# Performance work log

Measured on AMD Instinct MI355X. Metric: run time of the kernel, lower is better.

The kernel has to match this reference:

```python
import jax, jax.numpy as jnp
import numpy as np


def setup_inputs() -> dict:
    key = jax.random.key(0)
    k1, k2 = jax.random.split(key)
    B, Cin, H, W = 32, 32, 128, 128
    Cout, K = 64, 3
    inp = jax.random.normal(k1, (B, Cin, H, W), dtype=jnp.float32)
    # Original stores out_c*in_c*k*k scalar params; equivalent dense weight [Cout, Cin, K, K]
    kernel = jax.random.normal(k2, (Cout, Cin, K, K), dtype=jnp.float32)
    return {"input": inp, "kernel": kernel}


def reference(input, kernel):
    # Stride-1 cross-correlation with 'same' zero padding of (K-1)//2, identical
    # to the nested-loop slice/multiply/sum in the torch module.
    K = kernel.shape[-1]
    pad = (K - 1) // 2
    out = jax.lax.conv_general_dilated(
        input, kernel,
        window_strides=(1, 1),
        padding=[(pad, pad), (pad, pad)],
        dimension_numbers=("NCHW", "OIHW", "NCHW"),
    )
    return out  # [B, Cout, H, W]
```

## Files before the change

### kernel.cpp

```cpp
#include <hip/hip_runtime.h>
#include <hip/hip_bf16.h>
#include <stdint.h>

typedef short bf16x8 __attribute__((ext_vector_type(8)));
typedef float f32x4  __attribute__((ext_vector_type(4)));

#define B_   32
#define CIN  32
#define COUT 64
#define H_   128
#define W_   128
#define HW   (H_ * W_)
#define T_   2
#define RROWS 4
#define PXW  130
#define SCW  68

#define WAIT_LGKM0() __builtin_amdgcn_s_waitcnt(0xC07F)

static __device__ __forceinline__ ushort f2bf(float v) {
    __hip_bfloat16 h = __float2bfloat16(v);
    return __builtin_bit_cast(ushort, h);
}

__global__ void prep_w_kernel(const float* __restrict__ wt, ushort* __restrict__ Wp) {
    int p = blockIdx.x * blockDim.x + threadIdx.x;
    if (p >= COUT * CIN * 9) return;
    int j    = p & 7;
    int lane = (p >> 3) & 63;
    int g    = (p >> 9) & 3;
    int tap  = p >> 11;
    int oc   = g * 16 + (lane & 15);
    int cin  = (lane >> 4) * 8 + j;
    int ky   = tap / 3;
    int kx   = tap % 3;
    Wp[p] = f2bf(wt[(((size_t)oc * CIN + cin) * 3 + ky) * 3 + kx]);
}

__global__ __launch_bounds__(256, 4) void conv_fused_kernel(
    const float* __restrict__ in, const ushort* __restrict__ Wp,
    float* __restrict__ out) {
    __shared__ ushort lds[RROWS * PXW * 32];

    int hw_blk  = blockIdx.x;
    int logical = (hw_blk & 7) * 256 + (hw_blk >> 3);
    int b   = logical >> 6;
    int h0  = (logical & 63) * T_;
    int tid = threadIdx.x;

    for (int i = tid; i < RROWS * PXW; i += 256) {
        int r  = i / PXW;
        int px = i - r * PXW;
        int gy = h0 + r - 1;
        bf16x8 v[4];
        if (gy >= 0 && gy < H_ && px >= 1 && px <= W_) {
            const float* src = in + ((size_t)b * CIN * H_ + gy) * W_ + (px - 1);
#pragma unroll
            for (int q = 0; q < 4; ++q)
#pragma unroll
                for (int j = 0; j < 8; ++j)
                    v[q][j] = (short)f2bf(src[(size_t)(q * 8 + j) * HW]);
        } else {
#pragma unroll
            for (int q = 0; q < 4; ++q)
#pragma unroll
                for (int j = 0; j < 8; ++j)
                    v[q][j] = 0;
        }
        uint32_t base_byte = (uint32_t)i * 64;
        uint32_t sw = ((uint32_t)(px >> 1) & 3u) << 4;
#pragma unroll
        for (int q = 0; q < 4; ++q)
            *(bf16x8*)((char*)lds + base_byte + (((uint32_t)q << 4) ^ sw)) = v[q];
    }
    __syncthreads();

    int wid  = tid >> 6;
    int lane = tid & 63;
    int llo  = lane & 15;
    int lhi  = lane >> 4;
    int row  = wid >> 1;
    int px0  = (wid & 1) * 64;
    int h    = h0 + row;

    f32x4 acc[4][4];
#pragma unroll
    for (int g = 0; g < 4; ++g)
#pragma unroll
        for (int nf = 0; nf < 4; ++nf) {
            acc[g][nf][0] = 0.f; acc[g][nf][1] = 0.f;
            acc[g][nf][2] = 0.f; acc[g][nf][3] = 0.f;
        }

#pragma unroll
    for (int tap = 0; tap < 9; ++tap) {
        int dy = tap / 3;
        int dx = tap % 3;
        int rbase = (row + dy) * PXW;
        bf16x8 Af[4];
#pragma unroll
        for (int g = 0; g < 4; ++g)
            Af[g] = *(const bf16x8*)(Wp + ((size_t)(tap * 4 + g) * 64 + lane) * 8);
#pragma unroll
        for (int nf = 0; nf < 4; ++nf) {
            int px = px0 + nf * 16 + llo + dx;
            uint32_t byte = (uint32_t)(rbase + px) * 64u +
                            (((uint32_t)lhi << 4) ^ ((((uint32_t)px >> 1) & 3u) << 4));
            bf16x8 Bf = *(const bf16x8*)((const char*)lds + byte);
#pragma unroll
            for (int g = 0; g < 4; ++g)
                acc[g][nf] = __builtin_amdgcn_mfma_f32_16x16x32_bf16(Af[g], Bf, acc[g][nf], 0, 0, 0);
        }
    }

    __syncthreads();

    float* myscr = (float*)lds + wid * 16 * SCW;
    float* obase = out + (size_t)b * COUT * HW + (size_t)h * W_ + px0;
#pragma unroll
    for (int g = 0; g < 4; ++g) {
#pragma unroll
        for (int nf = 0; nf < 4; ++nf)
#pragma unroll
            for (int r = 0; r < 4; ++r)
                myscr[(lhi * 4 + r) * SCW + nf * 16 + llo] = acc[g][nf][r];
        WAIT_LGKM0();
#pragma unroll
        for (int j = 0; j < 4; ++j) {
            int ocp = j * 4 + lhi;
            f32x4 vv = *(const f32x4*)(myscr + ocp * SCW + llo * 4);
            int oc = g * 16 + ocp;
            *(f32x4*)(obase + (size_t)oc * HW + llo * 4) = vv;
        }
        WAIT_LGKM0();
    }
}

__global__ void conv_naive_kernel(const float* __restrict__ in,
                                  const float* __restrict__ wt,
                                  float* __restrict__ out) {
    int idx = blockIdx.x * blockDim.x + threadIdx.x;
    if (idx >= B_ * COUT * HW) return;
    int w  = idx & 127;
    int h  = (idx >> 7) & 127;
    int oc = (idx >> 14) & 63;
    int b  = idx >> 20;
    float s = 0.f;
    for (int c = 0; c < CIN; ++c)
        for (int ky = 0; ky < 3; ++ky) {
            int y = h + ky - 1;
            if ((unsigned)y >= (unsigned)H_) continue;
            for (int kx = 0; kx < 3; ++kx) {
                int x = w + kx - 1;
                if ((unsigned)x >= (unsigned)W_) continue;
                s += in[((size_t)(b * CIN + c) * H_ + y) * W_ + x] *
                     wt[(((size_t)oc * CIN + c) * 3 + ky) * 3 + kx];
            }
        }
    out[idx] = s;
}

extern "C" void kernel_launch(void* const* d_in, const int* in_sizes, int n_in,
                              void* d_out, int out_size, void* d_ws, size_t ws_size,
                              hipStream_t stream) {
    const float* in = (const float*)d_in[0];
    const float* wt = (const float*)d_in[1];
    float* out = (float*)d_out;

    size_t Wp_bytes = (size_t)COUT * CIN * 9 * 2;

    if (ws_size >= Wp_bytes) {
        ushort* Wp = (ushort*)d_ws;
        prep_w_kernel<<<(COUT * CIN * 9 + 255) / 256, 256, 0, stream>>>(wt, Wp);
        conv_fused_kernel<<<B_ * (H_ / T_), 256, 0, stream>>>(in, Wp, out);
    } else {
        int total = B_ * COUT * HW;
        conv_naive_kernel<<<(total + 255) / 256, 256, 0, stream>>>(in, wt, out);
    }
}
```

Measured before the change: 50.12 us.

## Give each wave a private LDS halo tile and drop block barriers

After: 51.84 us. +3.4%, slower.

```diff
diff --git a/kernel.cpp b/kernel.cpp
--- a/kernel.cpp
+++ b/kernel.cpp
@@ -11,9 +11,9 @@
 #define H_   128
 #define W_   128
 #define HW   (H_ * W_)
-#define T_   2
-#define RROWS 4
-#define PXW  130
+#define WCOLS 66
+#define WROWS 3
+#define WLDS  (WROWS * WCOLS * 32)
 #define SCW  68
 
 #define WAIT_LGKM0() __builtin_amdgcn_s_waitcnt(0xC07F)
@@ -37,51 +37,80 @@
     Wp[p] = f2bf(wt[(((size_t)oc * CIN + cin) * 3 + ky) * 3 + kx]);
 }
 
-__global__ __launch_bounds__(256, 4) void conv_fused_kernel(
+__global__ __launch_bounds__(256, 4) void conv_wave_kernel(
     const float* __restrict__ in, const ushort* __restrict__ Wp,
     float* __restrict__ out) {
-    __shared__ ushort lds[RROWS * PXW * 32];
+    __shared__ ushort lds[4 * WLDS];
 
     int hw_blk  = blockIdx.x;
     int logical = (hw_blk & 7) * 256 + (hw_blk >> 3);
-    int b   = logical >> 6;
-    int h0  = (logical & 63) * T_;
-    int tid = threadIdx.x;
-
-    for (int i = tid; i < RROWS * PXW; i += 256) {
-        int r  = i / PXW;
-        int px = i - r * PXW;
-        int gy = h0 + r - 1;
-        bf16x8 v[4];
-        if (gy >= 0 && gy < H_ && px >= 1 && px <= W_) {
-            const float* src = in + ((size_t)b * CIN * H_ + gy) * W_ + (px - 1);
-#pragma unroll
-            for (int q = 0; q < 4; ++q)
-#pragma unroll
-                for (int j = 0; j < 8; ++j)
-                    v[q][j] = (short)f2bf(src[(size_t)(q * 8 + j) * HW]);
-        } else {
-#pragma unroll
-            for (int q = 0; q < 4; ++q)
-#pragma unroll
-                for (int j = 0; j < 8; ++j)
-                    v[q][j] = 0;
-        }
-        uint32_t base_byte = (uint32_t)i * 64;
-        uint32_t sw = ((uint32_t)(px >> 1) & 3u) << 4;
-#pragma unroll
-        for (int q = 0; q < 4; ++q)
-            *(bf16x8*)((char*)lds + base_byte + (((uint32_t)q << 4) ^ sw)) = v[q];
-    }
-    __syncthreads();
-
+    int tid  = threadIdx.x;
     int wid  = tid >> 6;
     int lane = tid & 63;
     int llo  = lane & 15;
     int lhi  = lane >> 4;
-    int row  = wid >> 1;
-    int px0  = (wid & 1) * 64;
-    int h    = h0 + row;
+
+    int b   = logical >> 6;
+    int t   = (logical & 63) * 4 + wid;
+    int h   = t >> 1;
+    int px0 = (t & 1) * 64;
+
+    ushort* wlds = lds + wid * WLDS;
+    const float* ib = in + (size_t)b * CIN * HW;
+
+#pragma unroll
+    for (int r = 0; r < 3; ++r) {
+        int lc  = lane;
+        int gy  = h + r - 1;
+        int pxg = px0 + lc - 1;
+        bf16x8 v[4];
+        if (gy >= 0 && gy < H_ && pxg >= 0 && pxg < W_) {
+            const float* src = ib + (size_t)gy * W_ + pxg;
+#pragma unroll
+            for (int q = 0; q < 4; ++q)
+#pragma unroll
+                for (int j = 0; j < 8; ++j)
+                    v[q][j] = (short)f2bf(src[(size_t)(q * 8 + j) * HW]);
+        } else {
+#pragma unroll
+            for (int q = 0; q < 4; ++q)
+#pragma unroll
+                for (int j = 0; j < 8; ++j)
+                    v[q][j] = 0;
+        }
+        uint32_t base = (uint32_t)(r * WCOLS + lc) * 64u;
+        uint32_t sw = (((uint32_t)lc >> 1) & 3u) << 4;
+#pragma unroll
+        for (int q = 0; q < 4; ++q)
+            *(bf16x8*)((char*)wlds + base + (((uint32_t)q << 4) ^ sw)) = v[q];
+    }
+    if (lane < 6) {
+        int r   = lane >> 1;
+        int lc  = 64 + (lane & 1);
+        int gy  = h + r - 1;
+        int pxg = px0 + lc - 1;
+        bf16x8 v[4];
+        if (gy >= 0 && gy < H_ && pxg >= 0 && pxg < W_) {
+            const float* src = ib + (size_t)gy * W_ + pxg;
+#pragma unroll
+            for (int q = 0; q < 4; ++q)
+#pragma unroll
+                for (int j = 0; j < 8; ++j)
+                    v[q][j] = (short)f2bf(src[(size_t)(q * 8 + j) * HW]);
+        } else {
+#pragma unroll
+            for (int q = 0; q < 4; ++q)
+#pragma unroll
+                for (int j = 0; j < 8; ++j)
+                    v[q][j] = 0;
+        }
+        uint32_t base = (uint32_t)(r * WCOLS + lc) * 64u;
+        uint32_t sw = (((uint32_t)lc >> 1) & 3u) << 4;
+#pragma unroll
+        for (int q = 0; q < 4; ++q)
+            *(bf16x8*)((char*)wlds + base + (((uint32_t)q << 4) ^ sw)) = v[q];
+    }
+    WAIT_LGKM0();
 
     f32x4 acc[4][4];
 #pragma unroll
@@ -96,26 +125,23 @@
     for (int tap = 0; tap < 9; ++tap) {
         int dy = tap / 3;
         int dx = tap % 3;
-        int rbase = (row + dy) * PXW;
         bf16x8 Af[4];
 #pragma unroll
         for (int g = 0; g < 4; ++g)
             Af[g] = *(const bf16x8*)(Wp + ((size_t)(tap * 4 + g) * 64 + lane) * 8);
 #pragma unroll
         for (int nf = 0; nf < 4; ++nf) {
-            int px = px0 + nf * 16 + llo + dx;
-            uint32_t byte = (uint32_t)(rbase + px) * 64u +
-                            (((uint32_t)lhi << 4) ^ ((((uint32_t)px >> 1) & 3u) << 4));
-            bf16x8 Bf = *(const bf16x8*)((const char*)lds + byte);
+            int lc = nf * 16 + llo + dx;
+            uint32_t byte = (uint32_t)(dy * WCOLS + lc) * 64u +
+                            (((uint32_t)lhi << 4) ^ ((((uint32_t)lc >> 1) & 3u) << 4));
+            bf16x8 Bf = *(const bf16x8*)((const char*)wlds + byte);
 #pragma unroll
             for (int g = 0; g < 4; ++g)
                 acc[g][nf] = __builtin_amdgcn_mfma_f32_16x16x32_bf16(Af[g], Bf, acc[g][nf], 0, 0, 0);
         }
     }
 
-    __syncthreads();
-
-    float* myscr = (float*)lds + wid * 16 * SCW;
+    float* myscr = (float*)wlds;
     float* obase = out + (size_t)b * COUT * HW + (size_t)h * W_ + px0;
 #pragma unroll
     for (int g = 0; g < 4; ++g) {
@@ -172,7 +198,7 @@
     if (ws_size >= Wp_bytes) {
         ushort* Wp = (ushort*)d_ws;
         prep_w_kernel<<<(COUT * CIN * 9 + 255) / 256, 256, 0, stream>>>(wt, Wp);
-        conv_fused_kernel<<<B_ * (H_ / T_), 256, 0, stream>>>(in, Wp, out);
+        conv_wave_kernel<<<2048, 256, 0, stream>>>(in, Wp, out);
     } else {
         int total = B_ * COUT * HW;
         conv_naive_kernel<<<(total + 255) / 256, 256, 0, stream>>>(in, wt, out);
```
